# Kernel optimization log

Measured on AMD Instinct MI355X. Metric: run time of the kernel, lower is better.

Reference implementation:

```python
import jax, jax.numpy as jnp
import numpy as np

N, E, H, D, HD, L, G = 50000, 800000, 8, 16, 128, 6, 64
ND, ED, FF = 48, 4, 512


def _ln(x, g, b):
    m = x.mean(-1, keepdims=True)
    v = ((x - m) ** 2).mean(-1, keepdims=True)
    return (x - m) * jax.lax.rsqrt(v + 1e-5) * g + b


def setup_inputs() -> dict:
    key = jax.random.key(0)
    ks = iter(jax.random.split(key, 64))

    def rn(shape, s=0.05):
        return jax.random.normal(next(ks), shape, jnp.float32) * s

    inp = {
        "h": jax.random.normal(next(ks), (N, ND), jnp.float32),
        "e": jax.random.normal(next(ks), (E, ED), jnp.float32),
        "edge_index": jax.random.randint(next(ks), (2, E), 0, N),
        "batch": jnp.sort(jax.random.randint(next(ks), (N,), 0, G)),
        "node_W": rn((ND, HD)), "node_b": jnp.zeros(HD, jnp.float32),
        "edge_W": rn((ED, HD)), "edge_b": jnp.zeros(HD, jnp.float32),
        "Wq": rn((L, HD, HD)), "bq": jnp.zeros((L, HD), jnp.float32),
        "Wk": rn((L, HD, HD)), "bk": jnp.zeros((L, HD), jnp.float32),
        "Wv": rn((L, HD, HD)), "bv": jnp.zeros((L, HD), jnp.float32),
        "Wo": rn((L, HD, HD)), "bo": jnp.zeros((L, HD), jnp.float32),
        "Web": rn((L, HD, H)), "beb": jnp.zeros((L, H), jnp.float32),
        "W1": rn((L, HD, FF)), "b1": jnp.zeros((L, FF), jnp.float32),
        "W2": rn((L, FF, HD)), "b2": jnp.zeros((L, HD), jnp.float32),
        "g1": jnp.ones((L, HD), jnp.float32), "be1": jnp.zeros((L, HD), jnp.float32),
        "g2": jnp.ones((L, HD), jnp.float32), "be2": jnp.zeros((L, HD), jnp.float32),
        "gF": jnp.ones(HD, jnp.float32), "bF": jnp.zeros(HD, jnp.float32),
    }
    return inp


def reference(h, e, edge_index, batch, node_W, node_b, edge_W, edge_b,
              Wq, bq, Wk, bk, Wv, bv, Wo, bo, Web, beb,
              W1, b1, W2, b2, g1, be1, g2, be2, gF, bF):
    x = h @ node_W + node_b            # [N, HD]
    ee = e @ edge_W + edge_b           # [E, HD]
    row, col = edge_index[0], edge_index[1]
    n = x.shape[0]
    scale = 1.0 / np.sqrt(D).astype(np.float32)
    for l in range(L):
        res = x
        xn = _ln(x, g1[l], be1[l])
        q = (xn @ Wq[l] + bq[l]).reshape(n, H, D)
        k = (xn @ Wk[l] + bk[l]).reshape(n, H, D)
        v = (xn @ Wv[l] + bv[l]).reshape(n, H, D)
        # per-edge scores [E, H] with edge bias
        s = (q[row] * k[col]).sum(-1) * scale + (ee @ Web[l] + beb[l])
        # segment softmax over incoming edges of each row node
        mx = jax.ops.segment_max(s, row, num_segments=n)
        ex = jnp.exp(s - mx[row])
        den = jax.ops.segment_sum(ex, row, num_segments=n)[row] + 1e-10
        p = ex / den                   # [E, H]
        out = jax.ops.segment_sum(p[..., None] * v[col], row, num_segments=n)
        x = out.reshape(n, HD) @ Wo[l] + bo[l] + res
        res = x
        xn = _ln(x, g2[l], be2[l])
        x = jax.nn.relu(xn @ W1[l] + b1[l]) @ W2[l] + b2[l] + res
    x = _ln(x, gF, bF)
    cnt = jax.ops.segment_sum(jnp.ones((n,), x.dtype), batch, num_segments=G)
    gsum = jax.ops.segment_sum(x, batch, num_segments=G)
    graph_emb = gsum / jnp.maximum(cnt, 1.0)[:, None]
    return x, graph_emb
```

## Files before the change

### kernel.cpp

```cpp
#include <hip/hip_runtime.h>
#include <hip/hip_bf16.h>
#include <math.h>

#define NN 50000
#define EE 800000
#define HH 8
#define DD 16
#define HDIM 128
#define LL 6
#define GG 64
#define NDI 48
#define EDI 4
#define FFD 512
#define SCB ((NN + 1023) / 1024)

typedef __attribute__((ext_vector_type(8))) short short8;
typedef __attribute__((ext_vector_type(8))) unsigned short ushort8;
typedef __attribute__((ext_vector_type(4))) float floatx4;
typedef __attribute__((ext_vector_type(2))) float f32x2;

__device__ __forceinline__ unsigned short f2bf(float f) {
  unsigned u = __builtin_bit_cast(unsigned, f);
  unsigned rnd = 0x7FFFu + ((u >> 16) & 1u);
  return (unsigned short)((u + rnd) >> 16);
}
__device__ __forceinline__ float bf2f(unsigned short u) {
  unsigned v = ((unsigned)u) << 16;
  return __builtin_bit_cast(float, v);
}

#ifdef __has_builtin
#if __has_builtin(__builtin_amdgcn_cvt_pk_f32_fp8) && __has_builtin(__builtin_amdgcn_cvt_pk_fp8_f32)
#define HW_FP8 1
#endif
#endif

__device__ __forceinline__ unsigned char f2fp8(float f) {
#ifdef HW_FP8
  int p = __builtin_amdgcn_cvt_pk_fp8_f32(f, 0.f, 0, false);
  return (unsigned char)(p & 0xff);
#else
  unsigned u = __builtin_bit_cast(unsigned, f);
  unsigned s = (u >> 24) & 0x80u;
  unsigned au = u & 0x7fffffffu;
  float a = __builtin_bit_cast(float, au);
  if (a >= 448.f) return (unsigned char)(s | 0x7e);
  if (a < 0.0009765625f) return (unsigned char)s;
  int e32 = (int)(au >> 23) - 127;
  if (e32 >= -6) {
    au += (1u << 19);
    e32 = (int)(au >> 23) - 127;
    if (e32 > 8) return (unsigned char)(s | 0x7e);
    unsigned m = (au >> 20) & 7u;
    return (unsigned char)(s | (unsigned)((e32 + 7) << 3) | m);
  } else {
    int m = (int)(a * 512.f + 0.5f);
    if (m > 7) return (unsigned char)(s | 0x08);
    return (unsigned char)(s | (unsigned)m);
  }
#endif
}

__device__ __forceinline__ void fp8x8_dec(uint2 kw, float* f) {
#ifdef HW_FP8
  f32x2 a = __builtin_amdgcn_cvt_pk_f32_fp8((int)kw.x, false);
  f32x2 b = __builtin_amdgcn_cvt_pk_f32_fp8((int)kw.x, true);
  f32x2 c = __builtin_amdgcn_cvt_pk_f32_fp8((int)kw.y, false);
  f32x2 d = __builtin_amdgcn_cvt_pk_f32_fp8((int)kw.y, true);
  f[0] = a[0]; f[1] = a[1]; f[2] = b[0]; f[3] = b[1];
  f[4] = c[0]; f[5] = c[1]; f[6] = d[0]; f[7] = d[1];
#else
  unsigned w[2] = {kw.x, kw.y};
#pragma unroll
  for (int i = 0; i < 8; i++) {
    unsigned char bb = (unsigned char)((w[i >> 2] >> ((i & 3) * 8)) & 0xff);
    unsigned s = ((unsigned)bb & 0x80u) << 24;
    unsigned e = (bb >> 3) & 0xFu;
    unsigned m = bb & 7u;
    float v;
    if (e == 0) v = (float)m * 0.001953125f;
    else v = __builtin_bit_cast(float, ((e + 120u) << 23) | (m << 20));
    f[i] = __builtin_bit_cast(float, __builtin_bit_cast(unsigned, v) | s);
  }
#endif
}

__global__ void k_node_proj(const float* __restrict__ h, const float* __restrict__ W,
                            const float* __restrict__ b, float* __restrict__ x) {
  __shared__ float hs[32][NDI];
  int t = threadIdx.x;
  int n0 = blockIdx.x * 32;
  for (int idx = t; idx < 32 * NDI; idx += 128) {
    int nb = idx / NDI, i = idx - nb * NDI;
    int node = n0 + nb;
    hs[nb][i] = (node < NN) ? h[node * NDI + i] : 0.f;
  }
  __syncthreads();
  float acc[32];
#pragma unroll
  for (int nb = 0; nb < 32; nb++) acc[nb] = 0.f;
  for (int i = 0; i < NDI; i++) {
    float w = W[i * HDIM + t];
#pragma unroll
    for (int nb = 0; nb < 32; nb++) acc[nb] += hs[nb][i] * w;
  }
  float bb = b[t];
  for (int nb = 0; nb < 32; nb++) {
    int node = n0 + nb;
    if (node < NN) x[node * HDIM + t] = acc[nb] + bb;
  }
}

__global__ void k_pack(const float* __restrict__ W, unsigned short* __restrict__ dst,
                       int K, int OC, int nmat, float scale) {
  int KC = K >> 5, CT = OC >> 4;
  int total = nmat * CT * KC * 512;
  for (int i = blockIdx.x * 256 + threadIdx.x; i < total; i += gridDim.x * 256) {
    int j = i & 7;
    int lane = (i >> 3) & 63;
    int rest = i >> 9;
    int kc = rest % KC; rest /= KC;
    int ct = rest % CT; int m = rest / CT;
    int col = ct * 16 + (lane & 15);
    int k = kc * 32 + (lane >> 4) * 8 + j;
    dst[i] = f2bf(scale * W[(size_t)m * K * OC + (size_t)k * OC + col]);
  }
}

__global__ void k_wcomb(const float* __restrict__ edge_W, const float* __restrict__ edge_b,
                        const float* __restrict__ Web, const float* __restrict__ beb,
                        float* __restrict__ Wcomb, float* __restrict__ bcomb) {
  int t = threadIdx.x;
  if (t < LL * EDI * HH) {
    int l = t / (EDI * HH);
    int i = (t / HH) % EDI;
    int hh = t % HH;
    float s = 0.f;
    for (int j = 0; j < HDIM; j++) s += edge_W[i * HDIM + j] * Web[(l * HDIM + j) * HH + hh];
    Wcomb[t] = s;
  } else if (t < LL * EDI * HH + LL * HH) {
    int u = t - LL * EDI * HH;
    int l = u / HH, hh = u % HH;
    float s = beb[l * HH + hh];
    for (int j = 0; j < HDIM; j++) s += edge_b[j] * Web[(l * HDIM + j) * HH + hh];
    bcomb[u] = s;
  }
}

__global__ void k_deg(const int* __restrict__ row, int* __restrict__ deg) {
  int e = blockIdx.x * 256 + threadIdx.x;
  if (e < EE) atomicAdd(&deg[row[e]], 1);
}

__global__ void k_scan1(const int* __restrict__ deg, int* __restrict__ bsum) {
  __shared__ int red[256];
  int b = blockIdx.x, t = threadIdx.x;
  int base = b * 1024;
  int s = 0;
  for (int j = t; j < 1024; j += 256) {
    int i = base + j;
    s += (i < NN) ? deg[i] : 0;
  }
  red[t] = s;
  __syncthreads();
  for (int off = 128; off > 0; off >>= 1) {
    if (t < off) red[t] += red[t + off];
    __syncthreads();
  }
  if (t == 0) bsum[b] = red[0];
}

__global__ void k_scan2(int* __restrict__ bsum, int* __restrict__ starts) {
  if (threadIdx.x == 0) {
    int s = 0;
    for (int b = 0; b < SCB; b++) { int v = bsum[b]; bsum[b] = s; s += v; }
    starts[NN] = s;
  }
}

__global__ void k_scan3(const int* __restrict__ deg, const int* __restrict__ bsum,
                        int* __restrict__ starts, int* __restrict__ cursor) {
  __shared__ int tsum[256];
  int b = blockIdx.x, t = threadIdx.x;
  int base = b * 1024 + t * 4;
  int v[4];
  int s = 0;
#pragma unroll
  for (int j = 0; j < 4; j++) {
    int i = base + j;
    v[j] = (i < NN) ? deg[i] : 0;
    s += v[j];
  }
  tsum[t] = s;
  __syncthreads();
  for (int off = 1; off < 256; off <<= 1) {
    int xv = (t >= off) ? tsum[t - off] : 0;
    __syncthreads();
    tsum[t] += xv;
    __syncthreads();
  }
  int excl = tsum[t] - s + bsum[b];
#pragma unroll
  for (int j = 0; j < 4; j++) {
    int i = base + j;
    if (i < NN) { starts[i] = excl; cursor[i] = excl; excl += v[j]; }
  }
}

__global__ void k_scatter(const int* __restrict__ row, const int* __restrict__ col,
                          int* __restrict__ cursor,
                          int* __restrict__ eids, int* __restrict__ cols) {
  int e = blockIdx.x * 256 + threadIdx.x;
  if (e < EE) {
    int r = row[e];
    int pos = atomicAdd(&cursor[r], 1);
    eids[pos] = e;
    cols[pos] = col[e];
  }
}

__global__ void k_gbounds(const int* __restrict__ batch, int* __restrict__ gstart) {
  int i = blockIdx.x * 256 + threadIdx.x;
  if (i >= NN) return;
  int b = batch[i];
  int prev = (i == 0) ? -1 : batch[i - 1];
  for (int g = prev + 1; g <= b; g++) gstart[g] = i;
  if (i == NN - 1) {
    for (int g = b + 1; g <= GG; g++) gstart[g] = NN;
  }
}

__global__ void k_ebias(const int* __restrict__ eids, const float* __restrict__ efeat,
                        const float* __restrict__ Wcomb, const float* __restrict__ bcomb,
                        unsigned short* __restrict__ ebias) {
  int i = blockIdx.x * 256 + threadIdx.x;
  if (i >= EE) return;
  int e = eids[i];
  float4 ef = *(const float4*)(efeat + (size_t)e * EDI);
  ushort8 o;
#pragma unroll
  for (int hh = 0; hh < HH; hh++) {
    o[hh] = f2bf(bcomb[hh] + ef.x * Wcomb[hh] + ef.y * Wcomb[8 + hh] +
                 ef.z * Wcomb[16 + hh] + ef.w * Wcomb[24 + hh]);
  }
  *(ushort8*)(ebias + (size_t)i * 8) = o;
}

__global__ void k_ebias_all(const int* __restrict__ eids, const float* __restrict__ efeat,
                            const float* __restrict__ WcombAll,
                            const float* __restrict__ bcombAll,
                            unsigned short* __restrict__ ebias6) {
  int i = blockIdx.x * 256 + threadIdx.x;
  if (i >= EE) return;
  int e = eids[i];
  float4 ef = *(const float4*)(efeat + (size_t)e * EDI);
#pragma unroll
  for (int l = 0; l < LL; l++) {
    const float* Wc = WcombAll + l * 32;
    const float* bc = bcombAll + l * 8;
    ushort8 o;
#pragma unroll
    for (int hh = 0; hh < HH; hh++) {
      o[hh] = f2bf(bc[hh] + ef.x * Wc[hh] + ef.y * Wc[8 + hh] +
                   ef.z * Wc[16 + hh] + ef.w * Wc[24 + hh]);
    }
    *(ushort8*)(ebias6 + ((size_t)l * EE + i) * 8) = o;
  }
}

__global__ __launch_bounds__(256) void k_ln_qkv_mfma(
    const float* __restrict__ x,
    const unsigned short* __restrict__ Wqf, const float* __restrict__ bq,
    const unsigned short* __restrict__ Wkf, const float* __restrict__ bk,
    const unsigned short* __restrict__ Wvf, const float* __restrict__ bv,
    const float* __restrict__ g, const float* __restrict__ be,
    unsigned short* __restrict__ q, unsigned char* __restrict__ kf8,
    unsigned char* __restrict__ vf8) {
  __shared__ unsigned short xn[64][136];
  int t = threadIdx.x;
  int n0 = blockIdx.x * 64;
  {
    int row = t >> 2, quad = t & 3;
    int node = n0 + row;
    float xv[32];
    float s = 0.f, sq = 0.f;
    if (node < NN) {
      const float* xr = x + (size_t)node * HDIM + quad * 32;
#pragma unroll
      for (int c = 0; c < 8; c++) {
        float4 f = *(const float4*)(xr + c * 4);
        xv[c*4+0]=f.x; xv[c*4+1]=f.y; xv[c*4+2]=f.z; xv[c*4+3]=f.w;
      }
#pragma unroll
      for (int j = 0; j < 32; j++) { s += xv[j]; sq += xv[j]*xv[j]; }
    } else {
#pragma unroll
      for (int j = 0; j < 32; j++) xv[j] = 0.f;
    }
    s += __shfl_xor(s, 1); s += __shfl_xor(s, 2);
    sq += __shfl_xor(sq, 1); sq += __shfl_xor(sq, 2);
    float m = s * (1.f / HDIM);
    float rv = rsqrtf(sq * (1.f / HDIM) - m * m + 1e-5f);
#pragma unroll
    for (int cb = 0; cb < 4; cb++) {
      ushort8 u;
#pragma unroll
      for (int j = 0; j < 8; j++) {
        int col = quad * 32 + cb * 8 + j;
        u[j] = f2bf((xv[cb*8+j] - m) * rv * g[col] + be[col]);
      }
      *(ushort8*)&xn[row][quad * 32 + cb * 8] = u;
    }
  }
  __syncthreads();
  int w = t >> 6, lane = t & 63;
  int r0 = w * 16;
  short8 a[4];
#pragma unroll
  for (int kc = 0; kc < 4; kc++)
    a[kc] = *(const short8*)&xn[r0 + (lane & 15)][kc * 32 + (lane >> 4) * 8];
  const unsigned short* Wf[3] = {Wqf, Wkf, Wvf};
  const float* bias[3] = {bq, bk, bv};
#pragma unroll
  for (int mm = 0; mm < 3; mm++) {
    const unsigned short* wf = Wf[mm];
    float bscale = (mm == 0) ? 0.25f : 1.0f;
    for (int ct = 0; ct < 8; ct++) {
      floatx4 acc = {0.f, 0.f, 0.f, 0.f};
#pragma unroll
      for (int kc = 0; kc < 4; kc++) {
        short8 b = *(const short8*)(wf + ((size_t)(ct * 4 + kc) * 64 + lane) * 8);
        acc = __builtin_amdgcn_mfma_f32_16x16x32_bf16(a[kc], b, acc, 0, 0, 0);
      }
      int col = ct * 16 + (lane & 15);
      float bb = bias[mm][col] * bscale;
#pragma unroll
      for (int r = 0; r < 4; r++) {
        int rr = r0 + (lane >> 4) * 4 + r;
        int nd = n0 + rr;
        if (nd < NN) {
          float val = acc[r] + bb;
          if (mm == 0) q[(size_t)nd * HDIM + col] = f2bf(val);
          else if (mm == 1) kf8[(size_t)nd * HDIM + col] = f2fp8(val);
          else vf8[(size_t)nd * HDIM + col] = f2fp8(val);
        }
      }
    }
  }
}

__global__ __launch_bounds__(256) void k_attn(
    const unsigned short* __restrict__ q, const unsigned char* __restrict__ kf8,
    const unsigned char* __restrict__ vf8,
    const int* __restrict__ cols, const unsigned short* __restrict__ ebias,
    const int* __restrict__ starts,
    unsigned short* __restrict__ out) {
  int t = threadIdx.x;
  int wave = t >> 6, lane = t & 63;
  int g = lane >> 4, d = lane & 15;
  int node = blockIdx.x * 16 + wave * 4 + g;
  if (node >= NN) return;
  int hh = d >> 1;

  float qf[8];
  {
    ushort8 q8 = *(const ushort8*)(q + (size_t)node * HDIM + d * 8);
#pragma unroll
    for (int j = 0; j < 8; j++) qf[j] = bf2f(q8[j]);
  }

  int s0 = starts[node], s1 = starts[node + 1];
  float acc[8];
#pragma unroll
  for (int j = 0; j < 8; j++) acc[j] = 0.f;
  float lsum = 0.f;

  uint2 sk[4], sv[4];
  float seb[4];
  int pc[4];
  float peb[4];

#pragma unroll
  for (int j = 0; j < 4; j++) {
    int i = s0 + j;
    bool ok = i < s1;
    int c = ok ? cols[i] : 0;
    sk[j] = *(const uint2*)(kf8 + (size_t)c * HDIM + d * 8);
    sv[j] = *(const uint2*)(vf8 + (size_t)c * HDIM + d * 8);
    seb[j] = ok ? bf2f(ebias[(size_t)i * 8 + hh]) : -1e30f;
  }
#pragma unroll
  for (int j = 0; j < 4; j++) {
    int i = s0 + 4 + j;
    bool ok = i < s1;
    pc[j] = ok ? cols[i] : 0;
    peb[j] = ok ? bf2f(ebias[(size_t)i * 8 + hh]) : -1e30f;
  }

  for (int base = s0; base < s1; base += 4) {
#pragma unroll
    for (int j = 0; j < 4; j++) {
      int c = pc[j];
      uint2 kn = *(const uint2*)(kf8 + (size_t)c * HDIM + d * 8);
      uint2 vn = *(const uint2*)(vf8 + (size_t)c * HDIM + d * 8);
      float ebn = peb[j];
      int i2 = base + 8 + j;
      bool ok2 = i2 < s1;
      int c2 = ok2 ? cols[i2] : 0;
      float eb2 = ok2 ? bf2f(ebias[(size_t)i2 * 8 + hh]) : -1e30f;
      float kf[8], vf[8];
      fp8x8_dec(sk[j], kf);
      fp8x8_dec(sv[j], vf);
      float part = 0.f;
#pragma unroll
      for (int u = 0; u < 8; u++) part += qf[u] * kf[u];
      part += __shfl_xor(part, 1);
      float ex = __expf(part + seb[j]);
      lsum += ex;
#pragma unroll
      for (int u = 0; u < 8; u++) acc[u] += ex * vf[u];
      sk[j] = kn; sv[j] = vn; seb[j] = ebn;
      pc[j] = c2; peb[j] = eb2;
    }
  }

  float inv = 1.f / (lsum + 1e-10f);
  ushort8 o;
#pragma unroll
  for (int j = 0; j < 8; j++) o[j] = f2bf(acc[j] * inv);
  *(ushort8*)(out + (size_t)node * HDIM + d * 8) = o;
}

__global__ __launch_bounds__(256) void k_oproj_ffn(
    const unsigned short* __restrict__ ao, const unsigned short* __restrict__ Wof,
    const float* __restrict__ bo,
    const unsigned short* __restrict__ W1f, const float* __restrict__ b1,
    const unsigned short* __restrict__ W2f, const float* __restrict__ b2,
    const float* __restrict__ g, const float* __restrict__ be,
    float* __restrict__ x) {
  __shared__ unsigned short pool[32 * 536];
  unsigned short* aosp = pool;
  float* xrp = (float*)(pool + 8704);
  unsigned short* xnp = pool;
  int t = threadIdx.x;
  int n0 = blockIdx.x * 32;

#pragma unroll
  for (int c = 0; c < 2; c++) {
    int elem = c * 2048 + t * 8;
    int row = elem >> 7, col = elem & 127;
    int nd = n0 + row;
    ushort8 u = {0, 0, 0, 0, 0, 0, 0, 0};
    if (nd < NN) u = *(const ushort8*)(ao + (size_t)nd * HDIM + col);
    *(ushort8*)&aosp[row * 136 + col] = u;
  }
#pragma unroll
  for (int c = 0; c < 4; c++) {
    int elem = c * 1024 + t * 4;
    int row = elem >> 7, col = elem & 127;
    int nd = n0 + row;
    float4 f = {0.f, 0.f, 0.f, 0.f};
    if (nd < NN) f = *(const float4*)(x + (size_t)nd * HDIM + col);
    *(float4*)&xrp[row * 132 + col] = f;
  }
  __syncthreads();

  int w = t >> 6, lane = t & 63;
  int rt = w & 1, r0 = rt * 16;
  int cthalf = w >> 1;
  int lcol = lane & 15, lrow8 = (lane >> 4) * 8, lrow4 = (lane >> 4) * 4;

  float racc[4][4];
  {
    short8 a[4];
#pragma unroll
    for (int kc = 0; kc < 4; kc++)
      a[kc] = *(const short8*)&aosp[(r0 + lcol) * 136 + kc * 32 + lrow8];
#pragma unroll
    for (int ci = 0; ci < 4; ci++) {
      int ct = cthalf * 4 + ci;
      floatx4 acc = {0.f, 0.f, 0.f, 0.f};
#pragma unroll
      for (int kc = 0; kc < 4; kc++) {
        short8 b = *(const short8*)(Wof + ((size_t)(ct * 4 + kc) * 64 + lane) * 8);
        acc = __builtin_amdgcn_mfma_f32_16x16x32_bf16(a[kc], b, acc, 0, 0, 0);
      }
      int col = ct * 16 + lcol;
      float bb = bo[col];
#pragma unroll
      for (int r = 0; r < 4; r++) {
        int rr = r0 + lrow4 + r;
        float v = xrp[rr * 132 + col] + acc[r] + bb;
        racc[ci][r] = v;
        xrp[rr * 132 + col] = v;
      }
    }
  }
  __syncthreads();

  {
    int row = t >> 3, oct = t & 7;
    float xv[16];
    float s = 0.f, sq = 0.f;
#pragma unroll
    for (int jj = 0; jj < 16; jj++) {
      float f = xrp[row * 132 + oct * 16 + jj];
      xv[jj] = f; s += f; sq += f * f;
    }
    s += __shfl_xor(s, 1); s += __shfl_xor(s, 2); s += __shfl_xor(s, 4);
    sq += __shfl_xor(sq, 1); sq += __shfl_xor(sq, 2); sq += __shfl_xor(sq, 4);
    float m = s * (1.f / HDIM);
    float rv = rsqrtf(sq * (1.f / HDIM) - m * m + 1e-5f);
#pragma unroll
    for (int cb = 0; cb < 2; cb++) {
      ushort8 u;
#pragma unroll
      for (int jj = 0; jj < 8; jj++) {
        int col = oct * 16 + cb * 8 + jj;
        u[jj] = f2bf((xv[cb*8+jj] - m) * rv * g[col] + be[col]);
      }
      *(ushort8*)&xnp[row * 136 + oct * 16 + cb * 8] = u;
    }
  }
  __syncthreads();

  short8 axn[4];
#pragma unroll
  for (int kc = 0; kc < 4; kc++)
    axn[kc] = *(const short8*)&xnp[(r0 + lcol) * 136 + kc * 32 + lrow8];
  __syncthreads();

  for (int ci = 0; ci < 16; ci++) {
    int ct = cthalf * 16 + ci;
    floatx4 acc = {0.f, 0.f, 0.f, 0.f};
#pragma unroll
    for (int kc = 0; kc < 4; kc++) {
      short8 b = *(const short8*)(W1f + ((size_t)(ct * 4 + kc) * 64 + lane) * 8);
      acc = __builtin_amdgcn_mfma_f32_16x16x32_bf16(axn[kc], b, acc, 0, 0, 0);
    }
    int col = ct * 16 + lcol;
    float bb = b1[col];
#pragma unroll
    for (int r = 0; r < 4; r++) {
      pool[(r0 + lrow4 + r) * 536 + col] = f2bf(fmaxf(acc[r] + bb, 0.f));
    }
  }
  __syncthreads();

  {
    short8 ah[16];
#pragma unroll
    for (int kc = 0; kc < 16; kc++)
      ah[kc] = *(const short8*)&pool[(r0 + lcol) * 536 + kc * 32 + lrow8];
#pragma unroll
    for (int ci = 0; ci < 4; ci++) {
      int ct2 = cthalf * 4 + ci;
      floatx4 acc = {0.f, 0.f, 0.f, 0.f};
#pragma unroll
      for (int kc = 0; kc < 16; kc++) {
        short8 b = *(const short8*)(W2f + ((size_t)(ct2 * 16 + kc) * 64 + lane) * 8);
        acc = __builtin_amdgcn_mfma_f32_16x16x32_bf16(ah[kc], b, acc, 0, 0, 0);
      }
      int col = ct2 * 16 + lcol;
      float bb = b2[col];
#pragma unroll
      for (int r = 0; r < 4; r++) {
        int nd = n0 + r0 + lrow4 + r;
        if (nd < NN) x[(size_t)nd * HDIM + col] = racc[ci][r] + acc[r] + bb;
      }
    }
  }
}

__global__ __launch_bounds__(256) void k_final(
    const float* __restrict__ x, const float* __restrict__ g,
    const float* __restrict__ be, float* __restrict__ outx) {
  int t = threadIdx.x;
  int row = t >> 2, quad = t & 3;
  int node = blockIdx.x * 64 + row;
  if (node >= NN) return;
  const float* xr = x + (size_t)node * HDIM + quad * 32;
  float xv[32];
  float s = 0.f, sq = 0.f;
#pragma unroll
  for (int c = 0; c < 8; c++) {
    float4 f = *(const float4*)(xr + c * 4);
    xv[c*4+0]=f.x; xv[c*4+1]=f.y; xv[c*4+2]=f.z; xv[c*4+3]=f.w;
  }
#pragma unroll
  for (int j = 0; j < 32; j++) { s += xv[j]; sq += xv[j]*xv[j]; }
  s += __shfl_xor(s, 1); s += __shfl_xor(s, 2);
  sq += __shfl_xor(sq, 1); sq += __shfl_xor(sq, 2);
  float m = s * (1.f / HDIM);
  float rv = rsqrtf(sq * (1.f / HDIM) - m * m + 1e-5f);
  float* orow = outx + (size_t)node * HDIM + quad * 32;
#pragma unroll
  for (int c = 0; c < 8; c++) {
    float4 o;
    int col = quad * 32 + c * 4;
    o.x = (xv[c*4+0] - m) * rv * g[col+0] + be[col+0];
    o.y = (xv[c*4+1] - m) * rv * g[col+1] + be[col+1];
    o.z = (xv[c*4+2] - m) * rv * g[col+2] + be[col+2];
    o.w = (xv[c*4+3] - m) * rv * g[col+3] + be[col+3];
    *(float4*)(orow + c * 4) = o;
  }
}

__global__ void k_pool(const float* __restrict__ outx, const int* __restrict__ gstart,
                       float* __restrict__ outg) {
  __shared__ float part[4][HDIM];
  int g = blockIdx.x;
  int t = threadIdx.x;
  int hd = t & 127, p = t >> 7;
  int s0 = gstart[g];
  int c = gstart[g + 1] - s0;
  float s = 0.f;
  for (int i = p; i < c; i += 4) s += outx[(size_t)(s0 + i) * HDIM + hd];
  part[p][hd] = s;
  __syncthreads();
  if (p == 0) {
    float tot = part[0][hd] + part[1][hd] + part[2][hd] + part[3][hd];
    outg[g * HDIM + hd] = tot / fmaxf((float)c, 1.f);
  }
}

extern "C" void kernel_launch(void* const* d_in, const int* in_sizes, int n_in,
                              void* d_out, int out_size, void* d_ws, size_t ws_size,
                              hipStream_t stream) {
  const float* h      = (const float*)d_in[0];
  const float* e      = (const float*)d_in[1];
  const int*   eidx   = (const int*)d_in[2];
  const int*   batch  = (const int*)d_in[3];
  const float* node_W = (const float*)d_in[4];
  const float* node_b = (const float*)d_in[5];
  const float* edge_W = (const float*)d_in[6];
  const float* edge_b = (const float*)d_in[7];
  const float* Wq  = (const float*)d_in[8];
  const float* bq  = (const float*)d_in[9];
  const float* Wk  = (const float*)d_in[10];
  const float* bk  = (const float*)d_in[11];
  const float* Wv  = (const float*)d_in[12];
  const float* bv  = (const float*)d_in[13];
  const float* Wo  = (const float*)d_in[14];
  const float* bo  = (const float*)d_in[15];
  const float* Web = (const float*)d_in[16];
  const float* beb = (const float*)d_in[17];
  const float* W1  = (const float*)d_in[18];
  const float* b1  = (const float*)d_in[19];
  const float* W2  = (const float*)d_in[20];
  const float* b2  = (const float*)d_in[21];
  const float* g1  = (const float*)d_in[22];
  const float* be1 = (const float*)d_in[23];
  const float* g2  = (const float*)d_in[24];
  const float* be2 = (const float*)d_in[25];
  const float* gF  = (const float*)d_in[26];
  const float* bF  = (const float*)d_in[27];

  const int* rowArr = eidx;
  const int* colArr = eidx + EE;

  char* ws = (char*)d_ws;
  size_t off = 0;
  auto alloc = [&](size_t bytes) -> void* {
    void* p = ws + off;
    off = (off + bytes + 255) & ~(size_t)255;
    return p;
  };
  float* x    = (float*)alloc((size_t)NN * HDIM * 4);
  unsigned short* qb  = (unsigned short*)alloc((size_t)NN * HDIM * 2);
  unsigned char*  kf8 = (unsigned char*)alloc((size_t)NN * HDIM);
  unsigned char*  vf8 = (unsigned char*)alloc((size_t)NN * HDIM);
  unsigned short* ao  = (unsigned short*)alloc((size_t)NN * HDIM * 2);
  int* deg    = (int*)alloc((size_t)NN * 4);
  int* starts = (int*)alloc((size_t)(NN + 1) * 4);
  int* cursor = (int*)alloc((size_t)NN * 4);
  int* eids   = (int*)alloc((size_t)EE * 4);
  int* cols   = (int*)alloc((size_t)EE * 4);
  unsigned short* ebias = (unsigned short*)alloc((size_t)EE * HH * 2);
  int* bsum   = (int*)alloc((size_t)SCB * 4);
  float* Wcomb = (float*)alloc((size_t)LL * EDI * HH * 4);
  float* bcomb = (float*)alloc((size_t)LL * HH * 4);
  int* gstart = (int*)alloc((size_t)(GG + 1) * 4);
  const int QKV_FRAG = 8 * 4 * 512;
  const int FFN_FRAG1 = 32 * 4 * 512;
  const int FFN_FRAG2 = 8 * 16 * 512;
  unsigned short* Wqf = (unsigned short*)alloc((size_t)LL * QKV_FRAG * 2);
  unsigned short* Wkf = (unsigned short*)alloc((size_t)LL * QKV_FRAG * 2);
  unsigned short* Wvf = (unsigned short*)alloc((size_t)LL * QKV_FRAG * 2);
  unsigned short* Wof = (unsigned short*)alloc((size_t)LL * QKV_FRAG * 2);
  unsigned short* W1f = (unsigned short*)alloc((size_t)LL * FFN_FRAG1 * 2);
  unsigned short* W2f = (unsigned short*)alloc((size_t)LL * FFN_FRAG2 * 2);

  size_t need6 = (size_t)LL * EE * HH * 2;
  unsigned short* ebias6 = nullptr;
  if (off + need6 + 256 <= ws_size) ebias6 = (unsigned short*)alloc(need6);

  hipMemsetAsync(deg, 0, (size_t)NN * 4, stream);

  k_node_proj<<<(NN + 31) / 32, 128, 0, stream>>>(h, node_W, node_b, x);
  k_wcomb<<<1, 256, 0, stream>>>(edge_W, edge_b, Web, beb, Wcomb, bcomb);
  k_pack<<<(LL * QKV_FRAG + 255) / 256, 256, 0, stream>>>(Wq, Wqf, HDIM, HDIM, LL, 0.25f);
  k_pack<<<(LL * QKV_FRAG + 255) / 256, 256, 0, stream>>>(Wk, Wkf, HDIM, HDIM, LL, 1.0f);
  k_pack<<<(LL * QKV_FRAG + 255) / 256, 256, 0, stream>>>(Wv, Wvf, HDIM, HDIM, LL, 1.0f);
  k_pack<<<(LL * QKV_FRAG + 255) / 256, 256, 0, stream>>>(Wo, Wof, HDIM, HDIM, LL, 1.0f);
  k_pack<<<(LL * FFN_FRAG1 + 255) / 256, 256, 0, stream>>>(W1, W1f, HDIM, FFD, LL, 1.0f);
  k_pack<<<(LL * FFN_FRAG2 + 255) / 256, 256, 0, stream>>>(W2, W2f, FFD, HDIM, LL, 1.0f);
  k_deg<<<(EE + 255) / 256, 256, 0, stream>>>(rowArr, deg);
  k_scan1<<<SCB, 256, 0, stream>>>(deg, bsum);
  k_scan2<<<1, 64, 0, stream>>>(bsum, starts);
  k_scan3<<<SCB, 256, 0, stream>>>(deg, bsum, starts, cursor);
  k_scatter<<<(EE + 255) / 256, 256, 0, stream>>>(rowArr, colArr, cursor, eids, cols);
  k_gbounds<<<(NN + 255) / 256, 256, 0, stream>>>(batch, gstart);

  int nb64 = (NN + 63) / 64;
  int nb32 = (NN + 31) / 32;
  int nb16 = (NN + 15) / 16;
  int nbE  = (EE + 255) / 256;

  if (ebias6) {
    k_ebias_all<<<nbE, 256, 0, stream>>>(eids, e, Wcomb, bcomb, ebias6);
  }

  for (int l = 0; l < LL; l++) {
    k_ln_qkv_mfma<<<nb64, 256, 0, stream>>>(x,
        Wqf + (size_t)l * QKV_FRAG, bq + (size_t)l * HDIM,
        Wkf + (size_t)l * QKV_FRAG, bk + (size_t)l * HDIM,
        Wvf + (size_t)l * QKV_FRAG, bv + (size_t)l * HDIM,
        g1 + (size_t)l * HDIM, be1 + (size_t)l * HDIM, qb, kf8, vf8);
    const unsigned short* eb_l;
    if (ebias6) {
      eb_l = ebias6 + (size_t)l * EE * HH;
    } else {
      k_ebias<<<nbE, 256, 0, stream>>>(eids, e,
          Wcomb + (size_t)l * EDI * HH, bcomb + (size_t)l * HH, ebias);
      eb_l = ebias;
    }
    k_attn<<<nb16, 256, 0, stream>>>(qb, kf8, vf8, cols, eb_l, starts, ao);
    k_oproj_ffn<<<nb32, 256, 0, stream>>>(ao, Wof + (size_t)l * QKV_FRAG,
        bo + (size_t)l * HDIM,
        W1f + (size_t)l * FFN_FRAG1, b1 + (size_t)l * FFD,
        W2f + (size_t)l * FFN_FRAG2, b2 + (size_t)l * HDIM,
        g2 + (size_t)l * HDIM, be2 + (size_t)l * HDIM, x);
  }

  float* outx = (float*)d_out;
  float* outg = outx + (size_t)NN * HDIM;
  k_final<<<(NN + 63) / 64, 256, 0, stream>>>(x, gF, bF, outx);
  k_pool<<<GG, 512, 0, stream>>>(outx, gstart, outg);
}
```

Measured before the change: 1.080 ms.

## Fuse next layer's LN+QKV projection into oproj/FFN kernel epilogue

The layer-norm and Q/K/V projection for layer l+1 now run at the end of the out-projection/FFN kernel of layer l, reusing the same 32-node tile. The first layer's QKV keeps the standalone kernel. This removes one launch per layer and, in principle, the re-read of x, though the epilogue still reads x back from global memory after writing it. The fused kernel gains extra syncs, register pressure and more work per block, which may lower occupancy.

```diff
diff --git a/kernel.cpp b/kernel.cpp
--- a/kernel.cpp
+++ b/kernel.cpp
@@ -431,13 +431,20 @@
   *(ushort8*)(out + (size_t)node * HDIM + d * 8) = o;
 }
 
-__global__ __launch_bounds__(256) void k_oproj_ffn(
+__global__ __launch_bounds__(256) void k_oproj_ffn_qkv(
     const unsigned short* __restrict__ ao, const unsigned short* __restrict__ Wof,
     const float* __restrict__ bo,
     const unsigned short* __restrict__ W1f, const float* __restrict__ b1,
     const unsigned short* __restrict__ W2f, const float* __restrict__ b2,
     const float* __restrict__ g, const float* __restrict__ be,
-    float* __restrict__ x) {
+    float* __restrict__ x,
+    int doQKV,
+    const unsigned short* __restrict__ WqfN, const float* __restrict__ bqN,
+    const unsigned short* __restrict__ WkfN, const float* __restrict__ bkN,
+    const unsigned short* __restrict__ WvfN, const float* __restrict__ bvN,
+    const float* __restrict__ gN, const float* __restrict__ beN,
+    unsigned short* __restrict__ qOut, unsigned char* __restrict__ kf8Out,
+    unsigned char* __restrict__ vf8Out) {
   __shared__ unsigned short pool[32 * 536];
   unsigned short* aosp = pool;
   float* xrp = (float*)(pool + 8704);
@@ -567,6 +574,80 @@
       for (int r = 0; r < 4; r++) {
         int nd = n0 + r0 + lrow4 + r;
         if (nd < NN) x[(size_t)nd * HDIM + col] = racc[ci][r] + acc[r] + bb;
+      }
+    }
+  }
+
+  if (!doQKV) return;
+  __syncthreads();
+
+  if (t < 128) {
+    int row = t >> 2, quad = t & 3;
+    int node = n0 + row;
+    float xv[32];
+    float s = 0.f, sq = 0.f;
+    if (node < NN) {
+      const float* xr = x + (size_t)node * HDIM + quad * 32;
+#pragma unroll
+      for (int c = 0; c < 8; c++) {
+        float4 f = *(const float4*)(xr + c * 4);
+        xv[c*4+0]=f.x; xv[c*4+1]=f.y; xv[c*4+2]=f.z; xv[c*4+3]=f.w;
+      }
+#pragma unroll
+      for (int j = 0; j < 32; j++) { s += xv[j]; sq += xv[j]*xv[j]; }
+    } else {
+#pragma unroll
+      for (int j = 0; j < 32; j++) xv[j] = 0.f;
+    }
+    s += __shfl_xor(s, 1); s += __shfl_xor(s, 2);
+    sq += __shfl_xor(sq, 1); sq += __shfl_xor(sq, 2);
+    float m = s * (1.f / HDIM);
+    float rv = rsqrtf(sq * (1.f / HDIM) - m * m + 1e-5f);
+#pragma unroll
+    for (int cb = 0; cb < 4; cb++) {
+      ushort8 u;
+#pragma unroll
+      for (int j = 0; j < 8; j++) {
+        int col = quad * 32 + cb * 8 + j;
+        u[j] = f2bf((xv[cb*8+j] - m) * rv * gN[col] + beN[col]);
+      }
+      *(ushort8*)&xnp[row * 136 + quad * 32 + cb * 8] = u;
+    }
+  }
+  __syncthreads();
+
+  {
+    short8 a2[4];
+#pragma unroll
+    for (int kc = 0; kc < 4; kc++)
+      a2[kc] = *(const short8*)&xnp[(r0 + lcol) * 136 + kc * 32 + lrow8];
+    const unsigned short* Wf[3] = {WqfN, WkfN, WvfN};
+    const float* bias[3] = {bqN, bkN, bvN};
+#pragma unroll
+    for (int mm = 0; mm < 3; mm++) {
+      const unsigned short* wf = Wf[mm];
+      float bscale = (mm == 0) ? 0.25f : 1.0f;
+#pragma unroll
+      for (int ci = 0; ci < 4; ci++) {
+        int ct = cthalf * 4 + ci;
+        floatx4 acc = {0.f, 0.f, 0.f, 0.f};
+#pragma unroll
+        for (int kc = 0; kc < 4; kc++) {
+          short8 b = *(const short8*)(wf + ((size_t)(ct * 4 + kc) * 64 + lane) * 8);
+          acc = __builtin_amdgcn_mfma_f32_16x16x32_bf16(a2[kc], b, acc, 0, 0, 0);
+        }
+        int col = ct * 16 + lcol;
+        float bb = bias[mm][col] * bscale;
+#pragma unroll
+        for (int r = 0; r < 4; r++) {
+          int nd = n0 + r0 + lrow4 + r;
+          if (nd < NN) {
+            float val = acc[r] + bb;
+            if (mm == 0) qOut[(size_t)nd * HDIM + col] = f2bf(val);
+            else if (mm == 1) kf8Out[(size_t)nd * HDIM + col] = f2fp8(val);
+            else vf8Out[(size_t)nd * HDIM + col] = f2fp8(val);
+          }
+        }
       }
     }
   }
@@ -721,12 +802,10 @@
     k_ebias_all<<<nbE, 256, 0, stream>>>(eids, e, Wcomb, bcomb, ebias6);
   }
 
+  k_ln_qkv_mfma<<<nb64, 256, 0, stream>>>(x,
+      Wqf, bq, Wkf, bk, Wvf, bv, g1, be1, qb, kf8, vf8);
+
   for (int l = 0; l < LL; l++) {
-    k_ln_qkv_mfma<<<nb64, 256, 0, stream>>>(x,
-        Wqf + (size_t)l * QKV_FRAG, bq + (size_t)l * HDIM,
-        Wkf + (size_t)l * QKV_FRAG, bk + (size_t)l * HDIM,
-        Wvf + (size_t)l * QKV_FRAG, bv + (size_t)l * HDIM,
-        g1 + (size_t)l * HDIM, be1 + (size_t)l * HDIM, qb, kf8, vf8);
     const unsigned short* eb_l;
     if (ebias6) {
       eb_l = ebias6 + (size_t)l * EE * HH;
@@ -736,11 +815,18 @@
       eb_l = ebias;
     }
     k_attn<<<nb16, 256, 0, stream>>>(qb, kf8, vf8, cols, eb_l, starts, ao);
-    k_oproj_ffn<<<nb32, 256, 0, stream>>>(ao, Wof + (size_t)l * QKV_FRAG,
+    int ln = (l < LL - 1) ? (l + 1) : l;
+    k_oproj_ffn_qkv<<<nb32, 256, 0, stream>>>(ao, Wof + (size_t)l * QKV_FRAG,
         bo + (size_t)l * HDIM,
         W1f + (size_t)l * FFN_FRAG1, b1 + (size_t)l * FFD,
         W2f + (size_t)l * FFN_FRAG2, b2 + (size_t)l * HDIM,
-        g2 + (size_t)l * HDIM, be2 + (size_t)l * HDIM, x);
+        g2 + (size_t)l * HDIM, be2 + (size_t)l * HDIM, x,
+        (l < LL - 1) ? 1 : 0,
+        Wqf + (size_t)ln * QKV_FRAG, bq + (size_t)ln * HDIM,
+        Wkf + (size_t)ln * QKV_FRAG, bk + (size_t)ln * HDIM,
+        Wvf + (size_t)ln * QKV_FRAG, bv + (size_t)ln * HDIM,
+        g1 + (size_t)ln * HDIM, be1 + (size_t)ln * HDIM,
+        qb, kf8, vf8);
   }
 
   float* outx = (float*)d_out;
```

After: 1.225 ms. +13.4%, slower.
